# Performance work log

Hardware: AMD Instinct MI355X
Metric: run time of the kernel (lower is better)

## Reference

```python
import math
import jax, jax.numpy as jnp
import numpy as np

D, H, NB, L, K = 45, 256, 6, 2, 8          # features, hidden, maf blocks, made hidden layers, spline bins
M = 3 * K - 1                               # params per feature (tails='linear')
TAIL = -math.log(1e-6)                      # tail_bound = -log(alpha)
MIN_BW = MIN_BH = MIN_D = 1e-3


def _masks():
    # nflows MADE sequential degrees (random_mask=False)
    d_in = np.arange(1, D + 1)
    d_h = (np.arange(H) % (D - 1)) + 1
    m0 = (d_h[:, None] >= d_in[None, :]).astype(np.float32)   # [H, D]
    mh = (d_h[:, None] >= d_h[None, :]).astype(np.float32)    # [H, H]
    d_out = np.repeat(d_in, M)                                 # nflows tile(): each degree repeated M times
    mf = (d_out[:, None] > d_h[None, :]).astype(np.float32)   # [D*M, H], strict for output layer
    return jnp.asarray(m0), jnp.asarray(mh), jnp.asarray(mf)


def _rq_spline(x, params):
    # x: [B, D]; params: [B, D, M]. unconstrained_rational_quadratic_spline, tails='linear'.
    uw = params[..., :K] / math.sqrt(H)        # nflows divides by sqrt(hidden_features)
    uh = params[..., K:2 * K] / math.sqrt(H)
    const = math.log(math.exp(1.0 - MIN_D) - 1.0)
    ud = jnp.pad(params[..., 2 * K:], ((0, 0), (0, 0), (1, 1)), constant_values=const)  # [B,D,K+1]
    inside = (x >= -TAIL) & (x <= TAIL)
    xc = jnp.clip(x, -TAIL, TAIL)

    def bin_edges(u, mn):
        p = jax.nn.softmax(u, -1)
        p = mn + (1.0 - mn * K) * p
        c = jnp.pad(jnp.cumsum(p, -1), ((0, 0), (0, 0), (1, 0)))
        c = 2.0 * TAIL * c - TAIL
        c = c.at[..., 0].set(-TAIL).at[..., -1].set(TAIL)
        return c, c[..., 1:] - c[..., :-1]

    cw, w = bin_edges(uw, MIN_BW)              # cumwidths [B,D,K+1], widths [B,D,K]
    ch, h = bin_edges(uh, MIN_BH)
    d = MIN_D + jax.nn.softplus(ud)            # derivatives [B,D,K+1]

    idx = jnp.clip(jnp.sum((xc[..., None] >= cw), -1) - 1, 0, K - 1)[..., None]
    g = lambda a: jnp.take_along_axis(a, idx, -1)[..., 0]
    icw, ibw, ich, ih = g(cw[..., :-1]), g(w), g(ch[..., :-1]), g(h)
    idelta = g(h / w)
    id0, id1 = g(d[..., :-1]), g(d[..., 1:])

    th = (xc - icw) / ibw
    th1 = th * (1.0 - th)
    den = idelta + (id0 + id1 - 2.0 * idelta) * th1
    y = ich + ih * (idelta * th * th + id0 * th1) / den
    lad = jnp.log(idelta * idelta * (id1 * th * th + 2.0 * idelta * th1 + id0 * (1.0 - th) ** 2)) - 2.0 * jnp.log(den)
    return jnp.where(inside, y, x), jnp.where(inside, lad, 0.0)


def setup_inputs() -> dict:
    key = jax.random.key(0)
    ks = jax.random.split(key, 10)
    B, s = 32768, 0.02
    return {
        "x": jax.random.normal(ks[0], (B, D), jnp.float32),
        "cond": jax.random.normal(ks[1], (B, 1), jnp.float32),
        "W0": jax.random.normal(ks[2], (NB, H, D), jnp.float32) * s,
        "b0": jax.random.normal(ks[3], (NB, H), jnp.float32) * s,
        "Wc": jax.random.normal(ks[4], (NB, H, 1), jnp.float32) * s,
        "bc": jax.random.normal(ks[5], (NB, H), jnp.float32) * s,
        "Wh": jax.random.normal(ks[6], (NB, L, H, H), jnp.float32) * s,
        "bh": jax.random.normal(ks[7], (NB, L, H), jnp.float32) * s,
        "Wf": jax.random.normal(ks[8], (NB, D * M, H), jnp.float32) * s,
        "bf": jax.random.normal(ks[9], (NB, D * M), jnp.float32) * s,
    }


def reference(x, cond, W0, b0, Wc, bc, Wh, bh, Wf, bf):
    m0, mh, mf = _masks()
    z = x
    ld = jnp.zeros(x.shape[0], x.dtype)
    for b in range(NB):  # CompositeTransform of NB MAF blocks
        hid = z @ (W0[b] * m0).T + b0[b] + cond @ Wc[b].T + bc[b]
        for l in range(L):  # MaskedFeedforwardBlock: linear -> ReLU (dropout=0, no BN)
            hid = jax.nn.relu(hid @ (Wh[b, l] * mh).T + bh[b, l])
        params = (hid @ (Wf[b] * mf).T + bf[b]).reshape(z.shape[0], D, M)
        z, lad = _rq_spline(z, params)
        ld = ld + lad.sum(-1)
    log_z = 0.5 * D * math.log(2.0 * math.pi)
    return -0.5 * jnp.sum(z * z, axis=1) - log_z + ld
```

## Files before the change

kernel.cpp:

```cpp
#include <hip/hip_runtime.h>


typedef __bf16 bf16;
typedef __bf16 bf16x8 __attribute__((ext_vector_type(8)));
typedef float  f32x16 __attribute__((ext_vector_type(16)));

#define TAILF  13.815510557964274f
#define TAIL2  27.631021115928548f
#define CMIN   0.027631021115928548f
#define LOGZ   41.352233994210265f

#define WS_W0M   0
#define WS_WHM   196608
#define WS_WFM   1769472
#define WS_BEFF  5210112
#define WS_BFP   5216256
#define WS_WCC   5243136
#define WS_BHP   5249280
#define WS_NEED  5261568

#define N_W0  (6*256*64)
#define N_WH  (6*2*256*256)
#define N_WF  (6*5*224*256)
#define N_PREP (N_W0 + N_WH + N_WF)

__device__ __forceinline__ int s_deg(int s) {
    return (s < 216) ? (s / 6) : (36 + (s - 216) / 5);
}
__device__ __forceinline__ int s_orig(int s) {
    int d, rk;
    if (s < 216) { d = s / 6; rk = s - d * 6; }
    else { int u = s - 216; d = 36 + u / 5; rk = u - (u / 5) * 5; }
    return d + 44 * rk;
}

__global__ void prep_all(const float* __restrict__ W0, const float* __restrict__ b0,
                         const float* __restrict__ Wc, const float* __restrict__ bc,
                         const float* __restrict__ Wh, const float* __restrict__ Wf,
                         const float* __restrict__ bfv, const float* __restrict__ bh,
                         bf16* __restrict__ W0m, bf16* __restrict__ Whm,
                         bf16* __restrict__ Wfm,
                         float* __restrict__ beff, float* __restrict__ bfp,
                         float* __restrict__ Wcc, float* __restrict__ bhp)
{
    int idx = blockIdx.x * 256 + threadIdx.x;
    if (idx < N_W0) {
        int j = idx & 7, lane = (idx >> 3) & 63, chunk = idx >> 9;
        int kt = chunk & 3, cg = (chunk >> 2) & 7, b = chunk >> 5;
        int col = cg * 32 + (lane & 31);
        int k   = kt * 16 + (lane >> 5) * 8 + j;
        int o   = s_orig(col);
        float v = 0.f;
        if (k < 45 && s_deg(col) >= k)
            v = W0[(b * 256 + o) * 45 + k];
        W0m[idx] = (bf16)v;
        if (k == 0) {
            beff[b * 256 + col] = b0[b * 256 + o] + bc[b * 256 + o];
            Wcc[b * 256 + col]  = Wc[b * 256 + o];
        }
    } else if (idx < N_W0 + N_WH) {
        int id = idx - N_W0;
        int j = id & 7, lane = (id >> 3) & 63, chunk = id >> 9;
        int kt = chunk & 15, cg = (chunk >> 4) & 7, bl = chunk >> 7;
        int col = cg * 32 + (lane & 31);
        int k   = kt * 16 + (lane >> 5) * 8 + j;
        int oc  = s_orig(col), ok = s_orig(k);
        float v = (s_deg(col) >= s_deg(k)) ? Wh[bl * 65536 + oc * 256 + ok] : 0.f;
        Whm[id] = (bf16)v;
        if (k == 0)
            bhp[bl * 256 + col] = bh[bl * 256 + oc];
    } else if (idx < N_PREP) {
        int id = idx - (N_W0 + N_WH);
        int j = id & 7, lane = (id >> 3) & 63, chunk = id >> 9;
        int kt = chunk & 15, t2 = chunk >> 4;
        int cg = t2 % 7, bg = t2 / 7;
        int b  = bg / 5, g = bg - 5 * b;
        int col = cg * 32 + (lane & 31);
        int k   = kt * 16 + (lane >> 5) * 8 + j;
        int ok  = s_orig(k);
        int f   = 9 * g + col / 23;
        int m   = col - (col / 23) * 23;
        bool valid = (col < 207);
        float v = 0.f;
        if (valid && (f > s_deg(k)))
            v = Wf[(b * 1035 + f * 23 + m) * 256 + ok];
        Wfm[id] = (bf16)v;
        if (k == 0)
            bfp[bg * 224 + col] = valid ? bfv[b * 1035 + f * 23 + m] : 0.f;
    }
}

#define SO_ZF    0
#define SO_ZB    5888
#define SO_HIDA  9472
#define SO_PBUF  26368
#define SO_COND  40336
#define SO_LD    40464
#define SMEM_BYTES 40592

#define PBF 776

__constant__ unsigned char IN_NP[8]     = {1,1,1,1,1,1,2,2};
__constant__ unsigned char HID_NP[8]    = {2,3,3,5,6,6,8,8};
__constant__ unsigned char OUT_NP[5][7] = {
    {1,1,1,1,2,2,2},
    {2,3,3,3,3,4,4},
    {4,4,5,5,5,5,5},
    {6,6,6,6,7,7,7},
    {7,8,8,8,8,8,8}};

template<int MODE>
__device__ __forceinline__ void epi32(const f32x16& acc, int cg,
    const float* __restrict__ bias, const float* __restrict__ wcol,
    const float* condl, bf16* dst, int l31, int kh8)
{
    const int col = cg * 32 + l31;
    if (MODE == 2 && col >= 207) return;
    const float bv = bias[col];
    const int rb = kh8 >> 1;
    if (MODE == 2) {
        const int fl = col / 23, m = col - fl * 23;
        bf16* dp = dst + fl * PBF + m;
        #pragma unroll
        for (int r = 0; r < 16; ++r) {
            int row = (r & 3) + 8 * (r >> 2) + rb;
            dp[row * 24] = (bf16)(acc[r] + bv);
        }
    } else {
        const float wcv = (MODE == 0) ? wcol[col] : 0.f;
        #pragma unroll
        for (int r = 0; r < 16; ++r) {
            int row = (r & 3) + 8 * (r >> 2) + rb;
            float v = acc[r] + bv;
            if (MODE == 0) v += condl[row] * wcv;
            if (MODE == 1) v = fmaxf(v, 0.f);
            dst[row * 264 + col] = (bf16)v;
        }
    }
}

template<int KTFULL, int MODE>
__device__ __forceinline__ void gemm32r(
    const bf16* Asrc, const int lda,
    const bf16* __restrict__ Wp,
    const float* __restrict__ bias, const float* __restrict__ wcol,
    const float* condl, bf16* dst,
    int cg, int np,
    int lane, bool preEpiSync)
{
    const int l31 = lane & 31;
    const int kh8 = (lane >> 5) * 8;
    const bf16* Bp = Wp + (size_t)cg * (KTFULL * 512) + lane * 8;
    const bf16* Ap = Asrc + l31 * lda + kh8;

    f32x16 acc = {};
    bf16x8 rA0, rA1, rB0, rB1, rC0, rC1;

#define LB(c)  (*reinterpret_cast<const bf16x8*>(Bp + (size_t)(c) * 512))
#define LA(c)  (*reinterpret_cast<const bf16x8*>(Ap + (c) * 16))
#define CHUNK(breg, c) { \
    bf16x8 a_ = LA(c); \
    acc = __builtin_amdgcn_mfma_f32_32x32x16_bf16(a_, breg, acc, 0, 0, 0); }
#define LP(r0, r1, p) { r0 = LB(2*(p)); r1 = LB(2*(p)+1); }
#define CP(r0, r1, p) { CHUNK(r0, 2*(p)) CHUNK(r1, 2*(p)+1) }

    if (np > 0) {
        LP(rA0, rA1, 0);
        if (np > 1) LP(rB0, rB1, 1);
        if (np > 2) LP(rC0, rC1, 2);

        int p = 0;
        #pragma unroll 1
        while (p + 3 < np) {
            CP(rA0, rA1, p);
            LP(rA0, rA1, p + 3);
            CP(rB0, rB1, p + 1);
            if (p + 4 < np) LP(rB0, rB1, p + 4);
            CP(rC0, rC1, p + 2);
            if (p + 5 < np) LP(rC0, rC1, p + 5);
            p += 3;
        }
        CP(rA0, rA1, p);
        if (np - p > 1) CP(rB0, rB1, p + 1);
        if (np - p > 2) CP(rC0, rC1, p + 2);
    }

#undef LB
#undef LA
#undef CHUNK
#undef LP
#undef CP

    if (preEpiSync) __syncthreads();

    if (np > 0) epi32<MODE>(acc, cg, bias, wcol, condl, dst, l31, kh8);
    __syncthreads();
}

__device__ __forceinline__ void do_spline9(int fb, float* zf, bf16* zb,
                                           const bf16* pbuf, int t, float& lad_acc)
{
    if (t >= 288) return;
    const int fl = t >> 5, r = t & 31;
    const bf16* pp = pbuf + fl * PBF + r * 24;
    bf16x8 q0 = *reinterpret_cast<const bf16x8*>(pp);
    bf16x8 q1 = *reinterpret_cast<const bf16x8*>(pp + 8);
    bf16x8 q2 = *reinterpret_cast<const bf16x8*>(pp + 16);
    float P[23];
    #pragma unroll
    for (int m = 0; m < 8; ++m) P[m]      = (float)q0[m];
    #pragma unroll
    for (int m = 0; m < 8; ++m) P[8 + m]  = (float)q1[m];
    #pragma unroll
    for (int m = 0; m < 7; ++m) P[16 + m] = (float)q2[m];

    float xin = zf[r * 46 + fb + fl];
    float xc  = fminf(fmaxf(xin, -TAILF), TAILF);
    bool inside = (xin >= -TAILF) && (xin <= TAILF);

    float mw = P[0];
    #pragma unroll
    for (int i = 1; i < 8; ++i) mw = fmaxf(mw, P[i]);
    float ew[8], sw = 0.f;
    #pragma unroll
    for (int i = 0; i < 8; ++i) { ew[i] = __expf((P[i] - mw) * 0.0625f); sw += ew[i]; }
    float rws = TAIL2 * 0.992f / sw;
    float cw[9], wb[8];
    cw[0] = -TAILF;
    #pragma unroll
    for (int i = 0; i < 8; ++i) {
        wb[i] = fmaf(ew[i], rws, CMIN);
        cw[i + 1] = cw[i] + wb[i];
    }
    cw[8] = TAILF;
    wb[7] = TAILF - cw[7];

    float mh = P[8];
    #pragma unroll
    for (int i = 1; i < 8; ++i) mh = fmaxf(mh, P[8 + i]);
    float eh[8], sh = 0.f;
    #pragma unroll
    for (int i = 0; i < 8; ++i) { eh[i] = __expf((P[8 + i] - mh) * 0.0625f); sh += eh[i]; }
    float rhs = TAIL2 * 0.992f / sh;
    float ch[9], hb[8];
    ch[0] = -TAILF;
    #pragma unroll
    for (int i = 0; i < 8; ++i) {
        hb[i] = fmaf(eh[i], rhs, CMIN);
        ch[i + 1] = ch[i] + hb[i];
    }
    ch[8] = TAILF;
    hb[7] = TAILF - ch[7];

    float dd[9];
    dd[0] = 1.0f; dd[8] = 1.0f;
    #pragma unroll
    for (int i = 1; i < 8; ++i)
        dd[i] = 1e-3f + __logf(1.f + __expf(P[15 + i]));

    float icw = cw[0], ich = ch[0], ibw = wb[0], ibh = hb[0];
    float id0 = dd[0], id1 = dd[1];
    #pragma unroll
    for (int i = 1; i < 8; ++i) {
        bool ge = xc >= cw[i];
        icw = ge ? cw[i] : icw;  ich = ge ? ch[i] : ich;
        ibw = ge ? wb[i] : ibw;  ibh = ge ? hb[i] : ibh;
        id0 = ge ? dd[i] : id0;  id1 = ge ? dd[i + 1] : id1;
    }

    float th  = (xc - icw) / ibw;
    float th1 = th * (1.f - th);
    float dl  = ibh / ibw;
    float den = dl + (id0 + id1 - 2.f * dl) * th1;
    float yy  = ich + ibh * (dl * th * th + id0 * th1) / den;
    float num = dl * dl * (id1 * th * th + 2.f * dl * th1
                           + id0 * (1.f - th) * (1.f - th));
    float lad = __logf(num) - 2.f * __logf(den);

    if (inside) {
        zf[r * 46 + fb + fl] = yy;
        zb[r * 56 + fb + fl] = (bf16)yy;
    }
    lad_acc += inside ? lad : 0.f;
}

__global__ __launch_bounds__(512, 4) void maf_main(
    const float* __restrict__ x, const float* __restrict__ cond,
    const bf16* __restrict__ W0m, const bf16* __restrict__ Whm,
    const bf16* __restrict__ Wfm,
    const float* __restrict__ beff, const float* __restrict__ bfp,
    const float* __restrict__ Wcc, const float* __restrict__ bhp,
    float* __restrict__ out, int B)
{
    extern __shared__ char smem[];
    float* zf    = (float*)(smem + SO_ZF);
    bf16*  zb    = (bf16*)(smem + SO_ZB);
    bf16*  hidA  = (bf16*)(smem + SO_HIDA);
    bf16*  pbuf  = (bf16*)(smem + SO_PBUF);
    float* condl = (float*)(smem + SO_COND);
    float* ldl   = (float*)(smem + SO_LD);

    const int t    = threadIdx.x;
    const int r0   = blockIdx.x * 32;
    const int w    = t >> 6;
    const int lane = t & 63;
    const int wu   = __builtin_amdgcn_readfirstlane(w);

    for (int i = t; i < 32 * 11; i += 512) {
        int r = i / 11, c = i - (i / 11) * 11;
        zb[r * 56 + 45 + c] = (bf16)0.f;
    }
    if (t < 8) hidA[t] = (bf16)0.f;
    for (int i = t; i < 32 * 45; i += 512) {
        int r = i / 45, f = i - (i / 45) * 45;
        float v = (r0 + r < B) ? x[(size_t)(r0 + r) * 45 + f] : 0.f;
        zf[r * 46 + f] = v;
        zb[r * 56 + f] = (bf16)v;
    }
    if (t < 32) {
        condl[t] = (r0 + t < B) ? cond[r0 + t] : 0.f;
        ldl[t]   = 0.f;
    }
    __syncthreads();

    float lad_acc = 0.f;

    const int inNp  = IN_NP[wu];
    const int hidNp = HID_NP[wu];
    const int oNpOk = (wu < 7);

    #pragma unroll 1
    for (int b = 0; b < 6; ++b) {
        gemm32r<4, 0>(zb, 56, W0m + b * 16384,
                      beff + b * 256, Wcc + b * 256, condl,
                      hidA, wu, inNp, lane, false);
        #pragma unroll 1
        for (int l = 0; l < 2; ++l)
            gemm32r<16, 1>(hidA, 264, Whm + (b * 2 + l) * 65536,
                           bhp + (b * 2 + l) * 256, nullptr, condl,
                           hidA, wu, hidNp, lane, true);
        #pragma unroll 1
        for (int g = 0; g < 5; ++g) {
            gemm32r<16, 2>(hidA, 264, Wfm + (size_t)(b * 5 + g) * 57344,
                           bfp + (b * 5 + g) * 224, nullptr, condl,
                           pbuf, oNpOk ? wu : 0, oNpOk ? OUT_NP[g][wu] : 0,
                           lane, g > 0);
            do_spline9(g * 9, zf, zb, pbuf, t, lad_acc);
        }
        __syncthreads();
    }

    atomicAdd(&ldl[t & 31], lad_acc);
    __syncthreads();

    if (t < 32 && r0 + t < B) {
        float s = 0.f;
        #pragma unroll
        for (int f = 0; f < 45; ++f) { float v = zf[t * 46 + f]; s += v * v; }
        out[r0 + t] = -0.5f * s - LOGZ + ldl[t];
    }
}

extern "C" void kernel_launch(void* const* d_in, const int* in_sizes, int n_in,
                              void* d_out, int out_size, void* d_ws, size_t ws_size,
                              hipStream_t stream)
{
    const float* x    = (const float*)d_in[0];
    const float* cond = (const float*)d_in[1];
    const float* W0   = (const float*)d_in[2];
    const float* b0   = (const float*)d_in[3];
    const float* Wc   = (const float*)d_in[4];
    const float* bc   = (const float*)d_in[5];
    const float* Wh   = (const float*)d_in[6];
    const float* bh   = (const float*)d_in[7];
    const float* Wf   = (const float*)d_in[8];
    const float* bfv  = (const float*)d_in[9];
    float* out = (float*)d_out;

    const int B = in_sizes[0] / 45;
    if (ws_size < (size_t)WS_NEED) return;

    char* ws = (char*)d_ws;
    bf16*  W0m  = (bf16*)(ws + WS_W0M);
    bf16*  Whm  = (bf16*)(ws + WS_WHM);
    bf16*  Wfm  = (bf16*)(ws + WS_WFM);
    float* beff = (float*)(ws + WS_BEFF);
    float* bfp  = (float*)(ws + WS_BFP);
    float* Wcc  = (float*)(ws + WS_WCC);
    float* bhp  = (float*)(ws + WS_BHP);

    prep_all<<<(N_PREP + 255) / 256, 256, 0, stream>>>(
        W0, b0, Wc, bc, Wh, Wf, bfv, bh, W0m, Whm, Wfm, beff, bfp, Wcc, bhp);

    (void)hipFuncSetAttribute((const void*)maf_main,
                              hipFuncAttributeMaxDynamicSharedMemorySize,
                              SMEM_BYTES);

    const int nwg = (B + 31) / 32;
    maf_main<<<nwg, 512, SMEM_BYTES, stream>>>(
        x, cond, W0m, Whm, Wfm, beff, bfp, Wcc, bhp, out, B);
}
```

Measured before the change: 382.2 us.

## Process 128 rows per workgroup, reusing each weight fragment across four MFMA tiles

Each workgroup now processes 128 batch rows instead of 32. Every weight fragment loaded from global memory feeds four 32x32 MFMA accumulators, which cuts per-row weight traffic by four. LDS buffers, the spline task loop and the final reduction are resized to match, and launch bounds drop to one workgroup per CU. In exchange, LDS use grows to about 160 KB, limiting each CU to a single 8-wave workgroup with less latency hiding, register pressure rises, and there are fewer workgroups, which could leave CUs idle for small batches.

```diff
diff --git a/kernel.cpp b/kernel.cpp
--- a/kernel.cpp
+++ b/kernel.cpp
@@ -91,14 +91,14 @@
 }
 
 #define SO_ZF    0
-#define SO_ZB    5888
-#define SO_HIDA  9472
-#define SO_PBUF  26368
-#define SO_COND  40336
-#define SO_LD    40464
-#define SMEM_BYTES 40592
-
-#define PBF 776
+#define SO_ZB    23552
+#define SO_HIDA  37888
+#define SO_PBUF  105472
+#define SO_COND  160912
+#define SO_LD    161424
+#define SMEM_BYTES 161936
+
+#define PBF 3080
 
 __constant__ unsigned char IN_NP[8]     = {1,1,1,1,1,1,2,2};
 __constant__ unsigned char HID_NP[8]    = {2,3,3,5,6,6,8,8};
@@ -110,14 +110,14 @@
     {7,8,8,8,8,8,8}};
 
 template<int MODE>
-__device__ __forceinline__ void epi32(const f32x16& acc, int cg,
+__device__ __forceinline__ void epi32(const f32x16& acc, int cg, int tile,
     const float* __restrict__ bias, const float* __restrict__ wcol,
     const float* condl, bf16* dst, int l31, int kh8)
 {
     const int col = cg * 32 + l31;
     if (MODE == 2 && col >= 207) return;
     const float bv = bias[col];
-    const int rb = kh8 >> 1;
+    const int rb = (kh8 >> 1) + tile * 32;
     if (MODE == 2) {
         const int fl = col / 23, m = col - fl * 23;
         bf16* dp = dst + fl * PBF + m;
@@ -140,7 +140,7 @@
 }
 
 template<int KTFULL, int MODE>
-__device__ __forceinline__ void gemm32r(
+__device__ __forceinline__ void gemm128(
     const bf16* Asrc, const int lda,
     const bf16* __restrict__ Wp,
     const float* __restrict__ bias, const float* __restrict__ wcol,
@@ -151,16 +151,24 @@
     const int l31 = lane & 31;
     const int kh8 = (lane >> 5) * 8;
     const bf16* Bp = Wp + (size_t)cg * (KTFULL * 512) + lane * 8;
-    const bf16* Ap = Asrc + l31 * lda + kh8;
-
-    f32x16 acc = {};
+    const bf16* A0 = Asrc + l31 * lda + kh8;
+    const bf16* A1 = A0 + 32 * lda;
+    const bf16* A2 = A0 + 64 * lda;
+    const bf16* A3 = A0 + 96 * lda;
+
+    f32x16 acc0 = {}, acc1 = {}, acc2 = {}, acc3 = {};
     bf16x8 rA0, rA1, rB0, rB1, rC0, rC1;
 
 #define LB(c)  (*reinterpret_cast<const bf16x8*>(Bp + (size_t)(c) * 512))
-#define LA(c)  (*reinterpret_cast<const bf16x8*>(Ap + (c) * 16))
 #define CHUNK(breg, c) { \
-    bf16x8 a_ = LA(c); \
-    acc = __builtin_amdgcn_mfma_f32_32x32x16_bf16(a_, breg, acc, 0, 0, 0); }
+    bf16x8 a0_ = *reinterpret_cast<const bf16x8*>(A0 + (c) * 16); \
+    bf16x8 a1_ = *reinterpret_cast<const bf16x8*>(A1 + (c) * 16); \
+    bf16x8 a2_ = *reinterpret_cast<const bf16x8*>(A2 + (c) * 16); \
+    bf16x8 a3_ = *reinterpret_cast<const bf16x8*>(A3 + (c) * 16); \
+    acc0 = __builtin_amdgcn_mfma_f32_32x32x16_bf16(a0_, breg, acc0, 0, 0, 0); \
+    acc1 = __builtin_amdgcn_mfma_f32_32x32x16_bf16(a1_, breg, acc1, 0, 0, 0); \
+    acc2 = __builtin_amdgcn_mfma_f32_32x32x16_bf16(a2_, breg, acc2, 0, 0, 0); \
+    acc3 = __builtin_amdgcn_mfma_f32_32x32x16_bf16(a3_, breg, acc3, 0, 0, 0); }
 #define LP(r0, r1, p) { r0 = LB(2*(p)); r1 = LB(2*(p)+1); }
 #define CP(r0, r1, p) { CHUNK(r0, 2*(p)) CHUNK(r1, 2*(p)+1) }
 
@@ -186,105 +194,111 @@
     }
 
 #undef LB
-#undef LA
 #undef CHUNK
 #undef LP
 #undef CP
 
     if (preEpiSync) __syncthreads();
 
-    if (np > 0) epi32<MODE>(acc, cg, bias, wcol, condl, dst, l31, kh8);
+    if (np > 0) {
+        epi32<MODE>(acc0, cg, 0, bias, wcol, condl, dst, l31, kh8);
+        epi32<MODE>(acc1, cg, 1, bias, wcol, condl, dst, l31, kh8);
+        epi32<MODE>(acc2, cg, 2, bias, wcol, condl, dst, l31, kh8);
+        epi32<MODE>(acc3, cg, 3, bias, wcol, condl, dst, l31, kh8);
+    }
     __syncthreads();
 }
 
 __device__ __forceinline__ void do_spline9(int fb, float* zf, bf16* zb,
                                            const bf16* pbuf, int t, float& lad_acc)
 {
-    if (t >= 288) return;
-    const int fl = t >> 5, r = t & 31;
-    const bf16* pp = pbuf + fl * PBF + r * 24;
-    bf16x8 q0 = *reinterpret_cast<const bf16x8*>(pp);
-    bf16x8 q1 = *reinterpret_cast<const bf16x8*>(pp + 8);
-    bf16x8 q2 = *reinterpret_cast<const bf16x8*>(pp + 16);
-    float P[23];
-    #pragma unroll
-    for (int m = 0; m < 8; ++m) P[m]      = (float)q0[m];
-    #pragma unroll
-    for (int m = 0; m < 8; ++m) P[8 + m]  = (float)q1[m];
-    #pragma unroll
-    for (int m = 0; m < 7; ++m) P[16 + m] = (float)q2[m];
-
-    float xin = zf[r * 46 + fb + fl];
-    float xc  = fminf(fmaxf(xin, -TAILF), TAILF);
-    bool inside = (xin >= -TAILF) && (xin <= TAILF);
-
-    float mw = P[0];
-    #pragma unroll
-    for (int i = 1; i < 8; ++i) mw = fmaxf(mw, P[i]);
-    float ew[8], sw = 0.f;
-    #pragma unroll
-    for (int i = 0; i < 8; ++i) { ew[i] = __expf((P[i] - mw) * 0.0625f); sw += ew[i]; }
-    float rws = TAIL2 * 0.992f / sw;
-    float cw[9], wb[8];
-    cw[0] = -TAILF;
-    #pragma unroll
-    for (int i = 0; i < 8; ++i) {
-        wb[i] = fmaf(ew[i], rws, CMIN);
-        cw[i + 1] = cw[i] + wb[i];
-    }
-    cw[8] = TAILF;
-    wb[7] = TAILF - cw[7];
-
-    float mh = P[8];
-    #pragma unroll
-    for (int i = 1; i < 8; ++i) mh = fmaxf(mh, P[8 + i]);
-    float eh[8], sh = 0.f;
-    #pragma unroll
-    for (int i = 0; i < 8; ++i) { eh[i] = __expf((P[8 + i] - mh) * 0.0625f); sh += eh[i]; }
-    float rhs = TAIL2 * 0.992f / sh;
-    float ch[9], hb[8];
-    ch[0] = -TAILF;
-    #pragma unroll
-    for (int i = 0; i < 8; ++i) {
-        hb[i] = fmaf(eh[i], rhs, CMIN);
-        ch[i + 1] = ch[i] + hb[i];
-    }
-    ch[8] = TAILF;
-    hb[7] = TAILF - ch[7];
-
-    float dd[9];
-    dd[0] = 1.0f; dd[8] = 1.0f;
-    #pragma unroll
-    for (int i = 1; i < 8; ++i)
-        dd[i] = 1e-3f + __logf(1.f + __expf(P[15 + i]));
-
-    float icw = cw[0], ich = ch[0], ibw = wb[0], ibh = hb[0];
-    float id0 = dd[0], id1 = dd[1];
-    #pragma unroll
-    for (int i = 1; i < 8; ++i) {
-        bool ge = xc >= cw[i];
-        icw = ge ? cw[i] : icw;  ich = ge ? ch[i] : ich;
-        ibw = ge ? wb[i] : ibw;  ibh = ge ? hb[i] : ibh;
-        id0 = ge ? dd[i] : id0;  id1 = ge ? dd[i + 1] : id1;
-    }
-
-    float th  = (xc - icw) / ibw;
-    float th1 = th * (1.f - th);
-    float dl  = ibh / ibw;
-    float den = dl + (id0 + id1 - 2.f * dl) * th1;
-    float yy  = ich + ibh * (dl * th * th + id0 * th1) / den;
-    float num = dl * dl * (id1 * th * th + 2.f * dl * th1
-                           + id0 * (1.f - th) * (1.f - th));
-    float lad = __logf(num) - 2.f * __logf(den);
-
-    if (inside) {
-        zf[r * 46 + fb + fl] = yy;
-        zb[r * 56 + fb + fl] = (bf16)yy;
-    }
-    lad_acc += inside ? lad : 0.f;
-}
-
-__global__ __launch_bounds__(512, 4) void maf_main(
+    #pragma unroll 1
+    for (int task = t; task < 1152; task += 512) {
+        int fl = task >> 7, r = task & 127;
+        const bf16* pp = pbuf + fl * PBF + r * 24;
+        bf16x8 q0 = *reinterpret_cast<const bf16x8*>(pp);
+        bf16x8 q1 = *reinterpret_cast<const bf16x8*>(pp + 8);
+        bf16x8 q2 = *reinterpret_cast<const bf16x8*>(pp + 16);
+        float P[23];
+        #pragma unroll
+        for (int m = 0; m < 8; ++m) P[m]      = (float)q0[m];
+        #pragma unroll
+        for (int m = 0; m < 8; ++m) P[8 + m]  = (float)q1[m];
+        #pragma unroll
+        for (int m = 0; m < 7; ++m) P[16 + m] = (float)q2[m];
+
+        float xin = zf[r * 46 + fb + fl];
+        float xc  = fminf(fmaxf(xin, -TAILF), TAILF);
+        bool inside = (xin >= -TAILF) && (xin <= TAILF);
+
+        float mw = P[0];
+        #pragma unroll
+        for (int i = 1; i < 8; ++i) mw = fmaxf(mw, P[i]);
+        float ew[8], sw = 0.f;
+        #pragma unroll
+        for (int i = 0; i < 8; ++i) { ew[i] = __expf((P[i] - mw) * 0.0625f); sw += ew[i]; }
+        float rws = TAIL2 * 0.992f / sw;
+        float cw[9], wb[8];
+        cw[0] = -TAILF;
+        #pragma unroll
+        for (int i = 0; i < 8; ++i) {
+            wb[i] = fmaf(ew[i], rws, CMIN);
+            cw[i + 1] = cw[i] + wb[i];
+        }
+        cw[8] = TAILF;
+        wb[7] = TAILF - cw[7];
+
+        float mh = P[8];
+        #pragma unroll
+        for (int i = 1; i < 8; ++i) mh = fmaxf(mh, P[8 + i]);
+        float eh[8], sh = 0.f;
+        #pragma unroll
+        for (int i = 0; i < 8; ++i) { eh[i] = __expf((P[8 + i] - mh) * 0.0625f); sh += eh[i]; }
+        float rhs = TAIL2 * 0.992f / sh;
+        float ch[9], hb[8];
+        ch[0] = -TAILF;
+        #pragma unroll
+        for (int i = 0; i < 8; ++i) {
+            hb[i] = fmaf(eh[i], rhs, CMIN);
+            ch[i + 1] = ch[i] + hb[i];
+        }
+        ch[8] = TAILF;
+        hb[7] = TAILF - ch[7];
+
+        float dd[9];
+        dd[0] = 1.0f; dd[8] = 1.0f;
+        #pragma unroll
+        for (int i = 1; i < 8; ++i)
+            dd[i] = 1e-3f + __logf(1.f + __expf(P[15 + i]));
+
+        float icw = cw[0], ich = ch[0], ibw = wb[0], ibh = hb[0];
+        float id0 = dd[0], id1 = dd[1];
+        #pragma unroll
+        for (int i = 1; i < 8; ++i) {
+            bool ge = xc >= cw[i];
+            icw = ge ? cw[i] : icw;  ich = ge ? ch[i] : ich;
+            ibw = ge ? wb[i] : ibw;  ibh = ge ? hb[i] : ibh;
+            id0 = ge ? dd[i] : id0;  id1 = ge ? dd[i + 1] : id1;
+        }
+
+        float th  = (xc - icw) / ibw;
+        float th1 = th * (1.f - th);
+        float dl  = ibh / ibw;
+        float den = dl + (id0 + id1 - 2.f * dl) * th1;
+        float yy  = ich + ibh * (dl * th * th + id0 * th1) / den;
+        float num = dl * dl * (id1 * th * th + 2.f * dl * th1
+                               + id0 * (1.f - th) * (1.f - th));
+        float lad = __logf(num) - 2.f * __logf(den);
+
+        if (inside) {
+            zf[r * 46 + fb + fl] = yy;
+            zb[r * 56 + fb + fl] = (bf16)yy;
+        }
+        lad_acc += inside ? lad : 0.f;
+    }
+}
+
+__global__ __launch_bounds__(512, 1) void maf_main(
     const float* __restrict__ x, const float* __restrict__ cond,
     const bf16* __restrict__ W0m, const bf16* __restrict__ Whm,
     const bf16* __restrict__ Wfm,
@@ -301,23 +315,23 @@
     float* ldl   = (float*)(smem + SO_LD);
 
     const int t    = threadIdx.x;
-    const int r0   = blockIdx.x * 32;
+    const int r0   = blockIdx.x * 128;
     const int w    = t >> 6;
     const int lane = t & 63;
     const int wu   = __builtin_amdgcn_readfirstlane(w);
 
-    for (int i = t; i < 32 * 11; i += 512) {
+    for (int i = t; i < 128 * 11; i += 512) {
         int r = i / 11, c = i - (i / 11) * 11;
         zb[r * 56 + 45 + c] = (bf16)0.f;
     }
     if (t < 8) hidA[t] = (bf16)0.f;
-    for (int i = t; i < 32 * 45; i += 512) {
+    for (int i = t; i < 128 * 45; i += 512) {
         int r = i / 45, f = i - (i / 45) * 45;
         float v = (r0 + r < B) ? x[(size_t)(r0 + r) * 45 + f] : 0.f;
         zf[r * 46 + f] = v;
         zb[r * 56 + f] = (bf16)v;
     }
-    if (t < 32) {
+    if (t < 128) {
         condl[t] = (r0 + t < B) ? cond[r0 + t] : 0.f;
         ldl[t]   = 0.f;
     }
@@ -331,17 +345,17 @@
 
     #pragma unroll 1
     for (int b = 0; b < 6; ++b) {
-        gemm32r<4, 0>(zb, 56, W0m + b * 16384,
+        gemm128<4, 0>(zb, 56, W0m + b * 16384,
                       beff + b * 256, Wcc + b * 256, condl,
                       hidA, wu, inNp, lane, false);
         #pragma unroll 1
         for (int l = 0; l < 2; ++l)
-            gemm32r<16, 1>(hidA, 264, Whm + (b * 2 + l) * 65536,
+            gemm128<16, 1>(hidA, 264, Whm + (b * 2 + l) * 65536,
                            bhp + (b * 2 + l) * 256, nullptr, condl,
                            hidA, wu, hidNp, lane, true);
         #pragma unroll 1
         for (int g = 0; g < 5; ++g) {
-            gemm32r<16, 2>(hidA, 264, Wfm + (size_t)(b * 5 + g) * 57344,
+            gemm128<16, 2>(hidA, 264, Wfm + (size_t)(b * 5 + g) * 57344,
                            bfp + (b * 5 + g) * 224, nullptr, condl,
                            pbuf, oNpOk ? wu : 0, oNpOk ? OUT_NP[g][wu] : 0,
                            lane, g > 0);
@@ -350,10 +364,10 @@
         __syncthreads();
     }
 
-    atomicAdd(&ldl[t & 31], lad_acc);
+    atomicAdd(&ldl[t & 127], lad_acc);
     __syncthreads();
 
-    if (t < 32 && r0 + t < B) {
+    if (t < 128 && r0 + t < B) {
         float s = 0.f;
         #pragma unroll
         for (int f = 0; f < 45; ++f) { float v = zf[t * 46 + f]; s += v * v; }
@@ -396,7 +410,7 @@
                               hipFuncAttributeMaxDynamicSharedMemorySize,
                               SMEM_BYTES);
 
-    const int nwg = (B + 31) / 32;
+    const int nwg = (B + 127) / 128;
     maf_main<<<nwg, 512, SMEM_BYTES, stream>>>(
         x, cond, W0m, Whm, Wfm, beff, bfp, Wcc, bhp, out, B);
 }
```

New measurement: 356.8 us. 1.07x faster.
